# Optimization experiments

Measured on AMD Instinct MI355X. Metric: run time of the kernel, lower is better.

## Reference

```python
import math
import jax, jax.numpy as jnp
import numpy as np

N, T, D, H = 256, 128, 1024, 1024


def setup_inputs() -> dict:
    key = jax.random.key(0)
    k1, k2, k3, k4, k5 = jax.random.split(key, 5)
    x = jax.random.normal(k1, (N, T, D), dtype=jnp.float32)
    A = jax.random.normal(k2, (N, H, 4, 4), dtype=jnp.float32)
    Wx = jax.random.normal(k3, (D, 4 * H), dtype=jnp.float32) / math.sqrt(D)
    Wh = jax.random.normal(k4, (H, 4 * H), dtype=jnp.float32) / math.sqrt(H)
    Wattn = jax.random.normal(k5, (H, 4 * H), dtype=jnp.float32) / math.sqrt(H)
    b = jnp.zeros((4 * H,), dtype=jnp.float32)
    return {"x": x, "A": A, "Wx": Wx, "Wh": Wh, "Wattn": Wattn, "b": b}


def reference(x, A, Wx, Wh, Wattn, b):
    n, h = A.shape[0], A.shape[1]
    Af = A.reshape(n, h, 16)           # (N, H, 16) flattened 4x4 feature map
    h0 = Af.mean(axis=2)               # mean-pooled global feature inits h0, c0
    scale = 1.0 / math.sqrt(h)

    def step(carry, x_t):
        prev_h, prev_c = carry
        # scaled dot-product attention over 16 spatial locations
        logits = jnp.einsum("nh,nhl->nl", prev_h, Af) * scale   # (N, 16)
        w = jax.nn.softmax(logits, axis=1)
        attn = jnp.einsum("nhl,nl->nh", Af, w)                  # (N, H)
        # LSTM gates
        pre = x_t @ Wx + prev_h @ Wh + attn @ Wattn + b          # (N, 4H)
        i, f, o, g = jnp.split(pre, 4, axis=1)
        next_c = jax.nn.sigmoid(f) * prev_c + jax.nn.sigmoid(i) * jnp.tanh(g)
        next_h = jax.nn.sigmoid(o) * jnp.tanh(next_c)
        return (next_h, next_c), next_h

    xs = jnp.swapaxes(x, 0, 1)         # (T, N, D)
    _, hs = jax.lax.scan(step, (h0, h0), xs)
    return jnp.swapaxes(hs, 0, 1)      # (N, T, H)
```

## Files before the change

### kernel.cpp

```cpp
#include <hip/hip_runtime.h>
#include <hip/hip_bf16.h>

#define NB 256
#define TT 128
#define DD 1024
#define HH 1024
#define FH 4096
#define KTOT 3072

typedef __attribute__((ext_vector_type(4))) float f32x4;
typedef __attribute__((ext_vector_type(8))) short short8;

__device__ __forceinline__ unsigned short f2bf(float f) {
    union { float f; unsigned u; } v; v.f = f;
    unsigned u = v.u;
    u += 0x7FFFu + ((u >> 16) & 1u);
    return (unsigned short)(u >> 16);
}
__device__ __forceinline__ float bf2f(unsigned short u) {
    union { unsigned u; float f; } v; v.u = ((unsigned)u) << 16; return v.f;
}
__device__ __forceinline__ float sigm(float v) { return 1.f / (1.f + __expf(-v)); }
__device__ __forceinline__ float tanhf_(float v) { return 1.f - 2.f / (__expf(2.f * v) + 1.f); }

__device__ __forceinline__ void bmap(int bid, int& m0, int& j0) {
    int xx = bid & 7, yy = (bid >> 3) & 7, mt = bid >> 6;
    m0 = mt * 64;
    j0 = (xx * 8 + yy) * 16;
}

__device__ __forceinline__ short8 pack8(float4 v0, float4 v1) {
    short8 r;
    r[0] = (short)f2bf(v0.x); r[1] = (short)f2bf(v0.y);
    r[2] = (short)f2bf(v0.z); r[3] = (short)f2bf(v0.w);
    r[4] = (short)f2bf(v1.x); r[5] = (short)f2bf(v1.y);
    r[6] = (short)f2bf(v1.z); r[7] = (short)f2bf(v1.w);
    return r;
}

__global__ __launch_bounds__(256) void wt_prep(const float* __restrict__ Wx,
                                               const float* __restrict__ Wh,
                                               const float* __restrict__ Wattn,
                                               unsigned short* __restrict__ Wt) {
    __shared__ unsigned short tile[64][65];
    int k0 = blockIdx.x * 64;
    int c0 = blockIdx.y * 64;
    const float* src; int kl0;
    if (k0 < 1024)      { src = Wx;    kl0 = k0; }
    else if (k0 < 2048) { src = Wh;    kl0 = k0 - 1024; }
    else                { src = Wattn; kl0 = k0 - 2048; }
    int tid = threadIdx.x;
    int r = tid >> 2;
    int ch = (tid & 3) << 4;
    const float* p = src + (size_t)(kl0 + r) * FH + c0 + ch;
#pragma unroll
    for (int i = 0; i < 16; i += 4) {
        float4 v = *reinterpret_cast<const float4*>(p + i);
        tile[r][ch + i + 0] = f2bf(v.x);
        tile[r][ch + i + 1] = f2bf(v.y);
        tile[r][ch + i + 2] = f2bf(v.z);
        tile[r][ch + i + 3] = f2bf(v.w);
    }
    __syncthreads();
    alignas(16) unsigned short vals[16];
#pragma unroll
    for (int i = 0; i < 16; ++i) vals[i] = tile[ch + i][r];
    unsigned short* q = Wt + (size_t)(c0 + r) * KTOT + k0 + ch;
    *reinterpret_cast<uint4*>(q)     = *reinterpret_cast<uint4*>(&vals[0]);
    *reinterpret_cast<uint4*>(q + 8) = *reinterpret_cast<uint4*>(&vals[8]);
}

__global__ __launch_bounds__(256) void zero_buf(float* __restrict__ p, int n) {
    int i = blockIdx.x * 256 + threadIdx.x;
    if (i < n) p[i] = 0.f;
}

__global__ __launch_bounds__(256) void xconv(const float* __restrict__ x,
                                             unsigned short* __restrict__ xbf) {
    size_t i = ((size_t)blockIdx.x * 256 + threadIdx.x) * 8;
    float4 v0 = *reinterpret_cast<const float4*>(x + i);
    float4 v1 = *reinterpret_cast<const float4*>(x + i + 4);
    short8 p = pack8(v0, v1);
    *reinterpret_cast<short8*>(xbf + i) = p;
}

__global__ __launch_bounds__(256) void afT_prep(const float* __restrict__ A,
                                                unsigned short* __restrict__ AfT) {
    int n = blockIdx.x;
#pragma unroll
    for (int pass = 0; pass < 4; ++pass) {
        int hh = pass * 256 + threadIdx.x;
        const float4* p = reinterpret_cast<const float4*>(A + ((size_t)n * HH + hh) * 16);
        float4 a0 = p[0], a1 = p[1], a2 = p[2], a3 = p[3];
        float av[16] = {a0.x,a0.y,a0.z,a0.w, a1.x,a1.y,a1.z,a1.w,
                        a2.x,a2.y,a2.z,a2.w, a3.x,a3.y,a3.z,a3.w};
#pragma unroll
        for (int l = 0; l < 16; ++l)
            AfT[((size_t)n * 16 + l) * HH + hh] = f2bf(av[l]);
    }
}

__global__ __launch_bounds__(256) void g_gemm(const unsigned short* __restrict__ AfT,
                                              const unsigned short* __restrict__ Wt,
                                              unsigned short* __restrict__ G) {
    int n = blockIdx.y;
    int ct = blockIdx.x;
    int tid = threadIdx.x;
    int wv = tid >> 6, lane = tid & 63;
    int cw = lane & 15, k8 = (lane >> 4) << 3;
    const unsigned short* ap  = AfT + ((size_t)n * 16 + cw) * HH + k8;
    const unsigned short* bp0 = Wt + (size_t)(ct * 128 + wv * 32 + cw) * KTOT + 2048 + k8;
    const unsigned short* bp1 = Wt + (size_t)(ct * 128 + wv * 32 + 16 + cw) * KTOT + 2048 + k8;
    f32x4 acc0, acc1;
#pragma unroll
    for (int e = 0; e < 4; ++e) { acc0[e] = 0.f; acc1[e] = 0.f; }
#pragma unroll
    for (int ch = 0; ch < 32; ++ch) {
        short8 a  = *reinterpret_cast<const short8*>(ap  + ch * 32);
        short8 b0 = *reinterpret_cast<const short8*>(bp0 + ch * 32);
        short8 b1 = *reinterpret_cast<const short8*>(bp1 + ch * 32);
        acc0 = __builtin_amdgcn_mfma_f32_16x16x32_bf16(a, b0, acc0, 0, 0, 0);
        acc1 = __builtin_amdgcn_mfma_f32_16x16x32_bf16(a, b1, acc1, 0, 0, 0);
    }
    int r0 = (lane >> 4) << 2;
    int c0 = ct * 128 + wv * 32 + cw;
#pragma unroll
    for (int e = 0; e < 4; ++e) {
        int l = r0 + e;
        G[((size_t)n * FH + c0) * 16 + l]      = f2bf(acc0[e]);
        G[((size_t)n * FH + c0 + 16) * 16 + l] = f2bf(acc1[e]);
    }
}

__global__ __launch_bounds__(512) void init_kernel(const float* __restrict__ A,
                                                   float* __restrict__ c,
                                                   unsigned short* __restrict__ h0,
                                                   float* __restrict__ lg0) {
    int m0, j0; bmap(blockIdx.x, m0, j0);
    int tid = threadIdx.x;
    int r = tid >> 3, j2 = (tid & 7) * 2;
    int n = m0 + r;
    float lg[16];
#pragma unroll
    for (int l = 0; l < 16; ++l) lg[l] = 0.f;
#pragma unroll
    for (int e = 0; e < 2; ++e) {
        int j = j0 + j2 + e;
        const float4* p = reinterpret_cast<const float4*>(A + ((size_t)n * HH + j) * 16);
        float4 a0 = p[0], a1 = p[1], a2 = p[2], a3 = p[3];
        float av[16] = {a0.x,a0.y,a0.z,a0.w, a1.x,a1.y,a1.z,a1.w,
                        a2.x,a2.y,a2.z,a2.w, a3.x,a3.y,a3.z,a3.w};
        float s = 0.f;
#pragma unroll
        for (int l = 0; l < 16; ++l) s += av[l];
        float m = s * 0.0625f;
        c[(size_t)n * HH + j] = m;
        h0[(size_t)n * HH + j] = f2bf(m);
#pragma unroll
        for (int l = 0; l < 16; ++l) lg[l] += m * av[l];
    }
#pragma unroll
    for (int l = 0; l < 16; ++l) {
        lg[l] += __shfl_xor(lg[l], 1);
        lg[l] += __shfl_xor(lg[l], 2);
        lg[l] += __shfl_xor(lg[l], 4);
    }
    int l0 = (tid & 7) * 2;
    atomicAdd(&lg0[(size_t)n * 16 + l0],     lg[l0]);
    atomicAdd(&lg0[(size_t)n * 16 + l0 + 1], lg[l0 + 1]);
}

template<bool XBF>
__global__ __launch_bounds__(512)
void gemm_step(const float* __restrict__ x, const unsigned short* __restrict__ xbf,
               const unsigned short* __restrict__ hprev, unsigned short* __restrict__ hnext,
               const unsigned short* __restrict__ Wt, const unsigned short* __restrict__ G,
               const float* __restrict__ A, const float* __restrict__ bb,
               const float* __restrict__ lgcur, float* __restrict__ lgnext,
               float* __restrict__ lgz, float* __restrict__ c,
               float* __restrict__ out, int t) {
    __shared__ __attribute__((aligned(16))) char smem[131072];
    unsigned short* hsm = reinterpret_cast<unsigned short*>(smem);
    float* gsm = reinterpret_cast<float*>(smem);

    int m0, j0; bmap(blockIdx.x, m0, j0);
    int tid = threadIdx.x;
    int w = tid >> 6, lane = tid & 63;
    int wn = w & 1, wk = w >> 1;

    {
        int r = tid >> 3;
        const unsigned short* hp = hprev + (size_t)(m0 + r) * HH;
#pragma unroll
        for (int i = 0; i < 16; ++i) {
            int chunk = (tid & 7) + i * 8;
            int sw = chunk ^ (r & 7);
            *reinterpret_cast<uint4*>(&hsm[r * 1024 + sw * 8]) =
                *reinterpret_cast<const uint4*>(hp + chunk * 8);
        }
    }
    __syncthreads();

    int cw = lane & 15;
    int k8 = (lane >> 4) << 3;

    f32x4 acc[4][2];
#pragma unroll
    for (int mf = 0; mf < 4; ++mf)
#pragma unroll
        for (int fn = 0; fn < 2; ++fn)
#pragma unroll
            for (int e = 0; e < 4; ++e) acc[mf][fn][e] = 0.f;

    const unsigned short* bp[2];
#pragma unroll
    for (int fn = 0; fn < 2; ++fn) {
        int col = wn * 32 + fn * 16 + cw;
        int brow = (col >> 4) * 1024 + j0 + (col & 15);
        int kbase = (wk < 2) ? (wk * 512) : (1024 + (wk - 2) * 512);
        bp[fn] = Wt + (size_t)brow * KTOT + kbase + k8;
    }

    if (wk < 2) {
        if (XBF) {
            const unsigned short* ap[4];
#pragma unroll
            for (int mf = 0; mf < 4; ++mf)
                ap[mf] = xbf + ((size_t)(m0 + mf * 16 + cw) * TT + t) * DD + wk * 512 + k8;
#pragma unroll
            for (int ch = 0; ch < 16; ++ch) {
                short8 b0 = *reinterpret_cast<const short8*>(bp[0] + ch * 32);
                short8 b1 = *reinterpret_cast<const short8*>(bp[1] + ch * 32);
#pragma unroll
                for (int mf = 0; mf < 4; ++mf) {
                    short8 a = *reinterpret_cast<const short8*>(ap[mf] + ch * 32);
                    acc[mf][0] = __builtin_amdgcn_mfma_f32_16x16x32_bf16(a, b0, acc[mf][0], 0, 0, 0);
                    acc[mf][1] = __builtin_amdgcn_mfma_f32_16x16x32_bf16(a, b1, acc[mf][1], 0, 0, 0);
                }
            }
        } else {
            const float* ap[4];
#pragma unroll
            for (int mf = 0; mf < 4; ++mf)
                ap[mf] = x + ((size_t)(m0 + mf * 16 + cw) * TT + t) * DD + wk * 512 + k8;
#pragma unroll
            for (int ch = 0; ch < 16; ++ch) {
                short8 b0 = *reinterpret_cast<const short8*>(bp[0] + ch * 32);
                short8 b1 = *reinterpret_cast<const short8*>(bp[1] + ch * 32);
#pragma unroll
                for (int mf = 0; mf < 4; ++mf) {
                    float4 v0 = *reinterpret_cast<const float4*>(ap[mf] + ch * 32);
                    float4 v1 = *reinterpret_cast<const float4*>(ap[mf] + ch * 32 + 4);
                    short8 a = pack8(v0, v1);
                    acc[mf][0] = __builtin_amdgcn_mfma_f32_16x16x32_bf16(a, b0, acc[mf][0], 0, 0, 0);
                    acc[mf][1] = __builtin_amdgcn_mfma_f32_16x16x32_bf16(a, b1, acc[mf][1], 0, 0, 0);
                }
            }
        }
    } else {
        int kq = (wk - 2) * 512;
        int chunkBase = (kq + k8) >> 3;
#pragma unroll
        for (int ch = 0; ch < 16; ++ch) {
            short8 b0 = *reinterpret_cast<const short8*>(bp[0] + ch * 32);
            short8 b1 = *reinterpret_cast<const short8*>(bp[1] + ch * 32);
            int chunkI = chunkBase + ch * 4;
#pragma unroll
            for (int mf = 0; mf < 4; ++mf) {
                int row = mf * 16 + cw;
                int sw = chunkI ^ (row & 7);
                short8 a = *reinterpret_cast<const short8*>(&hsm[row * 1024 + sw * 8]);
                acc[mf][0] = __builtin_amdgcn_mfma_f32_16x16x32_bf16(a, b0, acc[mf][0], 0, 0, 0);
                acc[mf][1] = __builtin_amdgcn_mfma_f32_16x16x32_bf16(a, b1, acc[mf][1], 0, 0, 0);
            }
        }
    }

    __syncthreads();
    int r0 = (lane >> 4) << 2;
#pragma unroll
    for (int mf = 0; mf < 4; ++mf)
#pragma unroll
        for (int fn = 0; fn < 2; ++fn)
#pragma unroll
            for (int e = 0; e < 4; ++e)
                gsm[((size_t)wk * 64 + mf * 16 + r0 + e) * 68 + wn * 32 + fn * 16 + cw] =
                    acc[mf][fn][e];
    __syncthreads();

    int r = tid >> 3, j2 = (tid & 7) * 2;
    int n = m0 + r;

    float sm[16];
    {
        const float4* lp = reinterpret_cast<const float4*>(lgcur + (size_t)n * 16);
        float4 s0 = lp[0], s1 = lp[1], s2 = lp[2], s3 = lp[3];
        float s[16] = {s0.x,s0.y,s0.z,s0.w, s1.x,s1.y,s1.z,s1.w,
                       s2.x,s2.y,s2.z,s2.w, s3.x,s3.y,s3.z,s3.w};
        float mx = -1e30f;
#pragma unroll
        for (int l = 0; l < 16; ++l) { s[l] *= 0.03125f; mx = fmaxf(mx, s[l]); }
        float sum = 0.f;
#pragma unroll
        for (int l = 0; l < 16; ++l) { sm[l] = __expf(s[l] - mx); sum += sm[l]; }
        float inv = 1.f / sum;
#pragma unroll
        for (int l = 0; l < 16; ++l) sm[l] *= inv;
    }

    float pre[4][2];
#pragma unroll
    for (int g = 0; g < 4; ++g)
#pragma unroll
        for (int e = 0; e < 2; ++e) {
            int colL = g * 16 + j2 + e;
            float p = gsm[((size_t)0 * 64 + r) * 68 + colL]
                    + gsm[((size_t)1 * 64 + r) * 68 + colL]
                    + gsm[((size_t)2 * 64 + r) * 68 + colL]
                    + gsm[((size_t)3 * 64 + r) * 68 + colL];
            p += bb[g * HH + j0 + j2 + e];
            const unsigned short* gp = G + ((size_t)n * FH + g * HH + j0 + j2 + e) * 16;
            uint4 g0 = *reinterpret_cast<const uint4*>(gp);
            uint4 g1 = *reinterpret_cast<const uint4*>(gp + 8);
            const unsigned* gu = reinterpret_cast<const unsigned*>(&g0);
            float d = 0.f;
#pragma unroll
            for (int q = 0; q < 4; ++q) {
                d += sm[q * 2]     * bf2f((unsigned short)(gu[q] & 0xFFFF));
                d += sm[q * 2 + 1] * bf2f((unsigned short)(gu[q] >> 16));
            }
            const unsigned* gv = reinterpret_cast<const unsigned*>(&g1);
#pragma unroll
            for (int q = 0; q < 4; ++q) {
                d += sm[8 + q * 2]     * bf2f((unsigned short)(gv[q] & 0xFFFF));
                d += sm[8 + q * 2 + 1] * bf2f((unsigned short)(gv[q] >> 16));
            }
            pre[g][e] = p + d;
        }

    int j = j0 + j2;
    float2 cv = *reinterpret_cast<const float2*>(c + (size_t)n * HH + j);
    float hn[2], cn[2];
#pragma unroll
    for (int e = 0; e < 2; ++e) {
        float ig = sigm(pre[0][e]);
        float fg = sigm(pre[1][e]);
        float og = sigm(pre[2][e]);
        float gg = tanhf_(pre[3][e]);
        float cc = fg * (e ? cv.y : cv.x) + ig * gg;
        cn[e] = cc;
        hn[e] = og * tanhf_(cc);
    }
    *reinterpret_cast<float2*>(c + (size_t)n * HH + j) = make_float2(cn[0], cn[1]);
    unsigned hpack = (unsigned)f2bf(hn[0]) | ((unsigned)f2bf(hn[1]) << 16);
    *reinterpret_cast<unsigned*>(hnext + (size_t)n * HH + j) = hpack;
    *reinterpret_cast<float2*>(out + ((size_t)n * TT + t) * HH + j) = make_float2(hn[0], hn[1]);

    if ((blockIdx.x & 63) == 0) {
        int l0 = (tid & 7) * 2;
        lgz[(size_t)n * 16 + l0]     = 0.f;
        lgz[(size_t)n * 16 + l0 + 1] = 0.f;
    }

    float lg[16];
#pragma unroll
    for (int l = 0; l < 16; ++l) lg[l] = 0.f;
#pragma unroll
    for (int e = 0; e < 2; ++e) {
        const float4* p = reinterpret_cast<const float4*>(A + ((size_t)n * HH + j + e) * 16);
        float4 a0 = p[0], a1 = p[1], a2 = p[2], a3 = p[3];
        float av[16] = {a0.x,a0.y,a0.z,a0.w, a1.x,a1.y,a1.z,a1.w,
                        a2.x,a2.y,a2.z,a2.w, a3.x,a3.y,a3.z,a3.w};
        float hv = hn[e];
#pragma unroll
        for (int l = 0; l < 16; ++l) lg[l] += hv * av[l];
    }
#pragma unroll
    for (int l = 0; l < 16; ++l) {
        lg[l] += __shfl_xor(lg[l], 1);
        lg[l] += __shfl_xor(lg[l], 2);
        lg[l] += __shfl_xor(lg[l], 4);
    }
    int l0 = (tid & 7) * 2;
    atomicAdd(&lgnext[(size_t)n * 16 + l0],     lg[l0]);
    atomicAdd(&lgnext[(size_t)n * 16 + l0 + 1], lg[l0 + 1]);
}

extern "C" void kernel_launch(void* const* d_in, const int* in_sizes, int n_in,
                              void* d_out, int out_size, void* d_ws, size_t ws_size,
                              hipStream_t stream) {
    const float* x     = (const float*)d_in[0];
    const float* A     = (const float*)d_in[1];
    const float* Wx    = (const float*)d_in[2];
    const float* Wh    = (const float*)d_in[3];
    const float* Wattn = (const float*)d_in[4];
    const float* b     = (const float*)d_in[5];
    float* out = (float*)d_out;

    char* ws = (char*)d_ws;
    unsigned short* Wt   = (unsigned short*)(ws);
    unsigned short* G    = (unsigned short*)(ws + 25165824);
    unsigned short* AfT  = (unsigned short*)(ws + 58720256);
    unsigned short* hbuf = (unsigned short*)(ws + 67108864);
    float* c             = (float*)(ws + 68157440);
    float* lg            = (float*)(ws + 69206016);
    unsigned short* xbf  = (unsigned short*)(ws + 69255168);
    bool use_xbf = ws_size >= (size_t)69255168 + 67108864;

    wt_prep<<<dim3(48, 64), 256, 0, stream>>>(Wx, Wh, Wattn, Wt);
    zero_buf<<<48, 256, 0, stream>>>(lg, 3 * NB * 16);
    afT_prep<<<NB, 256, 0, stream>>>(A, AfT);
    g_gemm<<<dim3(32, NB), 256, 0, stream>>>(AfT, Wt, G);
    init_kernel<<<256, 512, 0, stream>>>(A, c, hbuf, lg);
    if (use_xbf) xconv<<<16384, 256, 0, stream>>>(x, xbf);

    for (int t = 0; t < TT; ++t) {
        const unsigned short* hp = hbuf + (size_t)(t & 1) * NB * HH;
        unsigned short* hx       = hbuf + (size_t)((t & 1) ^ 1) * NB * HH;
        float* lgc = lg + (size_t)(t % 3) * NB * 16;
        float* lgn = lg + (size_t)((t + 1) % 3) * NB * 16;
        float* lgzz = lg + (size_t)((t + 2) % 3) * NB * 16;
        if (use_xbf)
            gemm_step<true><<<256, 512, 0, stream>>>(x, xbf, hp, hx, Wt, G, A, b,
                                                     lgc, lgn, lgzz, c, out, t);
        else
            gemm_step<false><<<256, 512, 0, stream>>>(x, xbf, hp, hx, Wt, G, A, b,
                                                      lgc, lgn, lgzz, c, out, t);
    }
}
```

Before: 4.220 ms.

## Retile precompute GEMM and double per-step block threads with split-K LDS reduction

The attention-projection GEMM (g_gemm) is retiled to 128x128 output tiles per block with a 4x4 MFMA fragment grid per wave, instead of one batch row per block, so more operand data is reused per load and fewer blocks are launched. The per-timestep kernel moves from 512 to 1024 threads, each wave now covering a 32-row slice. The h operand is read directly from global memory instead of being staged in LDS, and the split-K partials are combined through a smaller LDS reduction buffer. The gate epilogue handles one column per thread. The aim is more latency hiding and shorter per-thread work on the sequential critical path, at the cost of more register pressure per block and uncached global reads of h.

```diff
diff --git a/kernel.cpp b/kernel.cpp
--- a/kernel.cpp
+++ b/kernel.cpp
@@ -103,32 +103,59 @@
 __global__ __launch_bounds__(256) void g_gemm(const unsigned short* __restrict__ AfT,
                                               const unsigned short* __restrict__ Wt,
                                               unsigned short* __restrict__ G) {
-    int n = blockIdx.y;
+    int mt = blockIdx.y;
     int ct = blockIdx.x;
     int tid = threadIdx.x;
-    int wv = tid >> 6, lane = tid & 63;
+    int w = tid >> 6, lane = tid & 63;
+    int wm = w >> 1, wn = w & 1;
     int cw = lane & 15, k8 = (lane >> 4) << 3;
-    const unsigned short* ap  = AfT + ((size_t)n * 16 + cw) * HH + k8;
-    const unsigned short* bp0 = Wt + (size_t)(ct * 128 + wv * 32 + cw) * KTOT + 2048 + k8;
-    const unsigned short* bp1 = Wt + (size_t)(ct * 128 + wv * 32 + 16 + cw) * KTOT + 2048 + k8;
-    f32x4 acc0, acc1;
-#pragma unroll
-    for (int e = 0; e < 4; ++e) { acc0[e] = 0.f; acc1[e] = 0.f; }
-#pragma unroll
+
+    const unsigned short* ap[4];
+    const unsigned short* bp[4];
+#pragma unroll
+    for (int mf = 0; mf < 4; ++mf)
+        ap[mf] = AfT + (size_t)(mt * 128 + wm * 64 + mf * 16 + cw) * HH + k8;
+#pragma unroll
+    for (int fn = 0; fn < 4; ++fn)
+        bp[fn] = Wt + (size_t)(ct * 128 + wn * 64 + fn * 16 + cw) * KTOT + 2048 + k8;
+
+    f32x4 acc[4][4];
+#pragma unroll
+    for (int mf = 0; mf < 4; ++mf)
+#pragma unroll
+        for (int fn = 0; fn < 4; ++fn)
+#pragma unroll
+            for (int e = 0; e < 4; ++e) acc[mf][fn][e] = 0.f;
+
+#pragma unroll 4
     for (int ch = 0; ch < 32; ++ch) {
-        short8 a  = *reinterpret_cast<const short8*>(ap  + ch * 32);
-        short8 b0 = *reinterpret_cast<const short8*>(bp0 + ch * 32);
-        short8 b1 = *reinterpret_cast<const short8*>(bp1 + ch * 32);
-        acc0 = __builtin_amdgcn_mfma_f32_16x16x32_bf16(a, b0, acc0, 0, 0, 0);
-        acc1 = __builtin_amdgcn_mfma_f32_16x16x32_bf16(a, b1, acc1, 0, 0, 0);
-    }
-    int r0 = (lane >> 4) << 2;
-    int c0 = ct * 128 + wv * 32 + cw;
-#pragma unroll
-    for (int e = 0; e < 4; ++e) {
-        int l = r0 + e;
-        G[((size_t)n * FH + c0) * 16 + l]      = f2bf(acc0[e]);
-        G[((size_t)n * FH + c0 + 16) * 16 + l] = f2bf(acc1[e]);
+        short8 a[4], b[4];
+#pragma unroll
+        for (int i = 0; i < 4; ++i)
+            a[i] = *reinterpret_cast<const short8*>(ap[i] + ch * 32);
+#pragma unroll
+        for (int i = 0; i < 4; ++i)
+            b[i] = *reinterpret_cast<const short8*>(bp[i] + ch * 32);
+#pragma unroll
+        for (int mf = 0; mf < 4; ++mf)
+#pragma unroll
+            for (int fn = 0; fn < 4; ++fn)
+                acc[mf][fn] = __builtin_amdgcn_mfma_f32_16x16x32_bf16(
+                    a[mf], b[fn], acc[mf][fn], 0, 0, 0);
+    }
+
+    int l0 = (lane >> 4) << 2;
+#pragma unroll
+    for (int mf = 0; mf < 4; ++mf) {
+        int n = mt * 8 + wm * 4 + mf;
+#pragma unroll
+        for (int fn = 0; fn < 4; ++fn) {
+            int cc = ct * 128 + wn * 64 + fn * 16 + cw;
+            unsigned lo = (unsigned)f2bf(acc[mf][fn][0]) | ((unsigned)f2bf(acc[mf][fn][1]) << 16);
+            unsigned hi = (unsigned)f2bf(acc[mf][fn][2]) | ((unsigned)f2bf(acc[mf][fn][3]) << 16);
+            uint2 val; val.x = lo; val.y = hi;
+            *reinterpret_cast<uint2*>(G + ((size_t)n * FH + cc) * 16 + l0) = val;
+        }
     }
 }
 
@@ -171,7 +198,7 @@
 }
 
 template<bool XBF>
-__global__ __launch_bounds__(512)
+__global__ __launch_bounds__(1024)
 void gemm_step(const float* __restrict__ x, const unsigned short* __restrict__ xbf,
                const unsigned short* __restrict__ hprev, unsigned short* __restrict__ hnext,
                const unsigned short* __restrict__ Wt, const unsigned short* __restrict__ G,
@@ -179,117 +206,115 @@
                const float* __restrict__ lgcur, float* __restrict__ lgnext,
                float* __restrict__ lgz, float* __restrict__ c,
                float* __restrict__ out, int t) {
-    __shared__ __attribute__((aligned(16))) char smem[131072];
-    unsigned short* hsm = reinterpret_cast<unsigned short*>(smem);
-    float* gsm = reinterpret_cast<float*>(smem);
-
+    __shared__ float red[2][64][68];
     int m0, j0; bmap(blockIdx.x, m0, j0);
     int tid = threadIdx.x;
     int w = tid >> 6, lane = tid & 63;
-    int wn = w & 1, wk = w >> 1;
-
-    {
-        int r = tid >> 3;
-        const unsigned short* hp = hprev + (size_t)(m0 + r) * HH;
-#pragma unroll
-        for (int i = 0; i < 16; ++i) {
-            int chunk = (tid & 7) + i * 8;
-            int sw = chunk ^ (r & 7);
-            *reinterpret_cast<uint4*>(&hsm[r * 1024 + sw * 8]) =
-                *reinterpret_cast<const uint4*>(hp + chunk * 8);
-        }
-    }
-    __syncthreads();
-
-    int cw = lane & 15;
-    int k8 = (lane >> 4) << 3;
-
-    f32x4 acc[4][2];
-#pragma unroll
-    for (int mf = 0; mf < 4; ++mf)
+    int wk = w & 3, wn = (w >> 2) & 1, wm = w >> 3;
+    int cw = lane & 15, k8 = (lane >> 4) << 3;
+
+    f32x4 acc[2][2];
+#pragma unroll
+    for (int mf = 0; mf < 2; ++mf)
 #pragma unroll
         for (int fn = 0; fn < 2; ++fn)
 #pragma unroll
             for (int e = 0; e < 4; ++e) acc[mf][fn][e] = 0.f;
 
     const unsigned short* bp[2];
+    int kbase = (wk < 2) ? wk * 512 : 1024 + (wk - 2) * 512;
 #pragma unroll
     for (int fn = 0; fn < 2; ++fn) {
         int col = wn * 32 + fn * 16 + cw;
         int brow = (col >> 4) * 1024 + j0 + (col & 15);
-        int kbase = (wk < 2) ? (wk * 512) : (1024 + (wk - 2) * 512);
         bp[fn] = Wt + (size_t)brow * KTOT + kbase + k8;
     }
 
     if (wk < 2) {
         if (XBF) {
-            const unsigned short* ap[4];
-#pragma unroll
-            for (int mf = 0; mf < 4; ++mf)
-                ap[mf] = xbf + ((size_t)(m0 + mf * 16 + cw) * TT + t) * DD + wk * 512 + k8;
-#pragma unroll
+            const unsigned short* ap[2];
+#pragma unroll
+            for (int mf = 0; mf < 2; ++mf)
+                ap[mf] = xbf + ((size_t)(m0 + wm * 32 + mf * 16 + cw) * TT + t) * DD
+                             + wk * 512 + k8;
+#pragma unroll 4
             for (int ch = 0; ch < 16; ++ch) {
+                short8 a0 = *reinterpret_cast<const short8*>(ap[0] + ch * 32);
+                short8 a1 = *reinterpret_cast<const short8*>(ap[1] + ch * 32);
                 short8 b0 = *reinterpret_cast<const short8*>(bp[0] + ch * 32);
                 short8 b1 = *reinterpret_cast<const short8*>(bp[1] + ch * 32);
-#pragma unroll
-                for (int mf = 0; mf < 4; ++mf) {
-                    short8 a = *reinterpret_cast<const short8*>(ap[mf] + ch * 32);
-                    acc[mf][0] = __builtin_amdgcn_mfma_f32_16x16x32_bf16(a, b0, acc[mf][0], 0, 0, 0);
-                    acc[mf][1] = __builtin_amdgcn_mfma_f32_16x16x32_bf16(a, b1, acc[mf][1], 0, 0, 0);
-                }
+                acc[0][0] = __builtin_amdgcn_mfma_f32_16x16x32_bf16(a0, b0, acc[0][0], 0, 0, 0);
+                acc[0][1] = __builtin_amdgcn_mfma_f32_16x16x32_bf16(a0, b1, acc[0][1], 0, 0, 0);
+                acc[1][0] = __builtin_amdgcn_mfma_f32_16x16x32_bf16(a1, b0, acc[1][0], 0, 0, 0);
+                acc[1][1] = __builtin_amdgcn_mfma_f32_16x16x32_bf16(a1, b1, acc[1][1], 0, 0, 0);
             }
         } else {
-            const float* ap[4];
-#pragma unroll
-            for (int mf = 0; mf < 4; ++mf)
-                ap[mf] = x + ((size_t)(m0 + mf * 16 + cw) * TT + t) * DD + wk * 512 + k8;
-#pragma unroll
+            const float* ap[2];
+#pragma unroll
+            for (int mf = 0; mf < 2; ++mf)
+                ap[mf] = x + ((size_t)(m0 + wm * 32 + mf * 16 + cw) * TT + t) * DD
+                           + wk * 512 + k8;
+#pragma unroll 2
             for (int ch = 0; ch < 16; ++ch) {
+                float4 u0 = *reinterpret_cast<const float4*>(ap[0] + ch * 32);
+                float4 u1 = *reinterpret_cast<const float4*>(ap[0] + ch * 32 + 4);
+                float4 v0 = *reinterpret_cast<const float4*>(ap[1] + ch * 32);
+                float4 v1 = *reinterpret_cast<const float4*>(ap[1] + ch * 32 + 4);
+                short8 a0 = pack8(u0, u1);
+                short8 a1 = pack8(v0, v1);
                 short8 b0 = *reinterpret_cast<const short8*>(bp[0] + ch * 32);
                 short8 b1 = *reinterpret_cast<const short8*>(bp[1] + ch * 32);
-#pragma unroll
-                for (int mf = 0; mf < 4; ++mf) {
-                    float4 v0 = *reinterpret_cast<const float4*>(ap[mf] + ch * 32);
-                    float4 v1 = *reinterpret_cast<const float4*>(ap[mf] + ch * 32 + 4);
-                    short8 a = pack8(v0, v1);
-                    acc[mf][0] = __builtin_amdgcn_mfma_f32_16x16x32_bf16(a, b0, acc[mf][0], 0, 0, 0);
-                    acc[mf][1] = __builtin_amdgcn_mfma_f32_16x16x32_bf16(a, b1, acc[mf][1], 0, 0, 0);
-                }
+                acc[0][0] = __builtin_amdgcn_mfma_f32_16x16x32_bf16(a0, b0, acc[0][0], 0, 0, 0);
+                acc[0][1] = __builtin_amdgcn_mfma_f32_16x16x32_bf16(a0, b1, acc[0][1], 0, 0, 0);
+                acc[1][0] = __builtin_amdgcn_mfma_f32_16x16x32_bf16(a1, b0, acc[1][0], 0, 0, 0);
+                acc[1][1] = __builtin_amdgcn_mfma_f32_16x16x32_bf16(a1, b1, acc[1][1], 0, 0, 0);
             }
         }
     } else {
-        int kq = (wk - 2) * 512;
-        int chunkBase = (kq + k8) >> 3;
-#pragma unroll
+        const unsigned short* ap[2];
+#pragma unroll
+        for (int mf = 0; mf < 2; ++mf)
+            ap[mf] = hprev + (size_t)(m0 + wm * 32 + mf * 16 + cw) * HH
+                          + (wk - 2) * 512 + k8;
+#pragma unroll 4
         for (int ch = 0; ch < 16; ++ch) {
+            short8 a0 = *reinterpret_cast<const short8*>(ap[0] + ch * 32);
+            short8 a1 = *reinterpret_cast<const short8*>(ap[1] + ch * 32);
             short8 b0 = *reinterpret_cast<const short8*>(bp[0] + ch * 32);
             short8 b1 = *reinterpret_cast<const short8*>(bp[1] + ch * 32);
-            int chunkI = chunkBase + ch * 4;
-#pragma unroll
-            for (int mf = 0; mf < 4; ++mf) {
-                int row = mf * 16 + cw;
-                int sw = chunkI ^ (row & 7);
-                short8 a = *reinterpret_cast<const short8*>(&hsm[row * 1024 + sw * 8]);
-                acc[mf][0] = __builtin_amdgcn_mfma_f32_16x16x32_bf16(a, b0, acc[mf][0], 0, 0, 0);
-                acc[mf][1] = __builtin_amdgcn_mfma_f32_16x16x32_bf16(a, b1, acc[mf][1], 0, 0, 0);
+            acc[0][0] = __builtin_amdgcn_mfma_f32_16x16x32_bf16(a0, b0, acc[0][0], 0, 0, 0);
+            acc[0][1] = __builtin_amdgcn_mfma_f32_16x16x32_bf16(a0, b1, acc[0][1], 0, 0, 0);
+            acc[1][0] = __builtin_amdgcn_mfma_f32_16x16x32_bf16(a1, b0, acc[1][0], 0, 0, 0);
+            acc[1][1] = __builtin_amdgcn_mfma_f32_16x16x32_bf16(a1, b1, acc[1][1], 0, 0, 0);
+        }
+    }
+
+    int r0 = (lane >> 4) << 2;
+    if (wk < 2) {
+#pragma unroll
+        for (int mf = 0; mf < 2; ++mf)
+#pragma unroll
+            for (int fn = 0; fn < 2; ++fn)
+                *reinterpret_cast<f32x4*>(
+                    &red[wk][wn * 32 + fn * 16 + cw][wm * 32 + mf * 16 + r0]) = acc[mf][fn];
+    }
+    __syncthreads();
+    if (wk >= 2) {
+#pragma unroll
+        for (int mf = 0; mf < 2; ++mf)
+#pragma unroll
+            for (int fn = 0; fn < 2; ++fn) {
+                float* p = &red[wk - 2][wn * 32 + fn * 16 + cw][wm * 32 + mf * 16 + r0];
+                f32x4 v = *reinterpret_cast<const f32x4*>(p);
+                v += acc[mf][fn];
+                *reinterpret_cast<f32x4*>(p) = v;
             }
-        }
-    }
-
+    }
     __syncthreads();
-    int r0 = (lane >> 4) << 2;
-#pragma unroll
-    for (int mf = 0; mf < 4; ++mf)
-#pragma unroll
-        for (int fn = 0; fn < 2; ++fn)
-#pragma unroll
-            for (int e = 0; e < 4; ++e)
-                gsm[((size_t)wk * 64 + mf * 16 + r0 + e) * 68 + wn * 32 + fn * 16 + cw] =
-                    acc[mf][fn][e];
-    __syncthreads();
-
-    int r = tid >> 3, j2 = (tid & 7) * 2;
+
+    int r = tid >> 4, j1 = tid & 15;
     int n = m0 + r;
+    int j = j0 + j1;
 
     float sm[16];
     {
@@ -308,82 +333,61 @@
         for (int l = 0; l < 16; ++l) sm[l] *= inv;
     }
 
-    float pre[4][2];
-#pragma unroll
-    for (int g = 0; g < 4; ++g)
-#pragma unroll
-        for (int e = 0; e < 2; ++e) {
-            int colL = g * 16 + j2 + e;
-            float p = gsm[((size_t)0 * 64 + r) * 68 + colL]
-                    + gsm[((size_t)1 * 64 + r) * 68 + colL]
-                    + gsm[((size_t)2 * 64 + r) * 68 + colL]
-                    + gsm[((size_t)3 * 64 + r) * 68 + colL];
-            p += bb[g * HH + j0 + j2 + e];
-            const unsigned short* gp = G + ((size_t)n * FH + g * HH + j0 + j2 + e) * 16;
-            uint4 g0 = *reinterpret_cast<const uint4*>(gp);
-            uint4 g1 = *reinterpret_cast<const uint4*>(gp + 8);
-            const unsigned* gu = reinterpret_cast<const unsigned*>(&g0);
-            float d = 0.f;
-#pragma unroll
-            for (int q = 0; q < 4; ++q) {
-                d += sm[q * 2]     * bf2f((unsigned short)(gu[q] & 0xFFFF));
-                d += sm[q * 2 + 1] * bf2f((unsigned short)(gu[q] >> 16));
-            }
-            const unsigned* gv = reinterpret_cast<const unsigned*>(&g1);
-#pragma unroll
-            for (int q = 0; q < 4; ++q) {
-                d += sm[8 + q * 2]     * bf2f((unsigned short)(gv[q] & 0xFFFF));
-                d += sm[8 + q * 2 + 1] * bf2f((unsigned short)(gv[q] >> 16));
-            }
-            pre[g][e] = p + d;
+    float pre[4];
+#pragma unroll
+    for (int g = 0; g < 4; ++g) {
+        int colL = g * 16 + j1;
+        float p = red[0][colL][r] + red[1][colL][r] + bb[g * HH + j];
+        const unsigned short* gp = G + ((size_t)n * FH + g * HH + j) * 16;
+        uint4 g0 = *reinterpret_cast<const uint4*>(gp);
+        uint4 g1 = *reinterpret_cast<const uint4*>(gp + 8);
+        const unsigned* gu = reinterpret_cast<const unsigned*>(&g0);
+        const unsigned* gv = reinterpret_cast<const unsigned*>(&g1);
+        float d = 0.f;
+#pragma unroll
+        for (int q = 0; q < 4; ++q) {
+            d += sm[q * 2]     * bf2f((unsigned short)(gu[q] & 0xFFFF));
+            d += sm[q * 2 + 1] * bf2f((unsigned short)(gu[q] >> 16));
         }
-
-    int j = j0 + j2;
-    float2 cv = *reinterpret_cast<const float2*>(c + (size_t)n * HH + j);
-    float hn[2], cn[2];
-#pragma unroll
-    for (int e = 0; e < 2; ++e) {
-        float ig = sigm(pre[0][e]);
-        float fg = sigm(pre[1][e]);
-        float og = sigm(pre[2][e]);
-        float gg = tanhf_(pre[3][e]);
-        float cc = fg * (e ? cv.y : cv.x) + ig * gg;
-        cn[e] = cc;
-        hn[e] = og * tanhf_(cc);
-    }
-    *reinterpret_cast<float2*>(c + (size_t)n * HH + j) = make_float2(cn[0], cn[1]);
-    unsigned hpack = (unsigned)f2bf(hn[0]) | ((unsigned)f2bf(hn[1]) << 16);
-    *reinterpret_cast<unsigned*>(hnext + (size_t)n * HH + j) = hpack;
-    *reinterpret_cast<float2*>(out + ((size_t)n * TT + t) * HH + j) = make_float2(hn[0], hn[1]);
-
-    if ((blockIdx.x & 63) == 0) {
-        int l0 = (tid & 7) * 2;
-        lgz[(size_t)n * 16 + l0]     = 0.f;
-        lgz[(size_t)n * 16 + l0 + 1] = 0.f;
-    }
+#pragma unroll
+        for (int q = 0; q < 4; ++q) {
+            d += sm[8 + q * 2]     * bf2f((unsigned short)(gv[q] & 0xFFFF));
+            d += sm[8 + q * 2 + 1] * bf2f((unsigned short)(gv[q] >> 16));
+        }
+        pre[g] = p + d;
+    }
+
+    float cv = c[(size_t)n * HH + j];
+    float ig = sigm(pre[0]);
+    float fg = sigm(pre[1]);
+    float og = sigm(pre[2]);
+    float gg = tanhf_(pre[3]);
+    float cn = fg * cv + ig * gg;
+    float hn = og * tanhf_(cn);
+    c[(size_t)n * HH + j] = cn;
+    hnext[(size_t)n * HH + j] = f2bf(hn);
+    out[((size_t)n * TT + t) * HH + j] = hn;
+
+    if ((blockIdx.x & 63) == 0)
+        lgz[(size_t)n * 16 + j1] = 0.f;
 
     float lg[16];
-#pragma unroll
-    for (int l = 0; l < 16; ++l) lg[l] = 0.f;
-#pragma unroll
-    for (int e = 0; e < 2; ++e) {
-        const float4* p = reinterpret_cast<const float4*>(A + ((size_t)n * HH + j + e) * 16);
+    {
+        const float4* p = reinterpret_cast<const float4*>(A + ((size_t)n * HH + j) * 16);
         float4 a0 = p[0], a1 = p[1], a2 = p[2], a3 = p[3];
-        float av[16] = {a0.x,a0.y,a0.z,a0.w, a1.x,a1.y,a1.z,a1.w,
-                        a2.x,a2.y,a2.z,a2.w, a3.x,a3.y,a3.z,a3.w};
-        float hv = hn[e];
-#pragma unroll
-        for (int l = 0; l < 16; ++l) lg[l] += hv * av[l];
+        lg[0]=hn*a0.x;  lg[1]=hn*a0.y;  lg[2]=hn*a0.z;  lg[3]=hn*a0.w;
+        lg[4]=hn*a1.x;  lg[5]=hn*a1.y;  lg[6]=hn*a1.z;  lg[7]=hn*a1.w;
+        lg[8]=hn*a2.x;  lg[9]=hn*a2.y;  lg[10]=hn*a2.z; lg[11]=hn*a2.w;
+        lg[12]=hn*a3.x; lg[13]=hn*a3.y; lg[14]=hn*a3.z; lg[15]=hn*a3.w;
     }
 #pragma unroll
     for (int l = 0; l < 16; ++l) {
         lg[l] += __shfl_xor(lg[l], 1);
         lg[l] += __shfl_xor(lg[l], 2);
         lg[l] += __shfl_xor(lg[l], 4);
-    }
-    int l0 = (tid & 7) * 2;
-    atomicAdd(&lgnext[(size_t)n * 16 + l0],     lg[l0]);
-    atomicAdd(&lgnext[(size_t)n * 16 + l0 + 1], lg[l0 + 1]);
+        lg[l] += __shfl_xor(lg[l], 8);
+    }
+    atomicAdd(&lgnext[(size_t)n * 16 + j1], lg[j1]);
 }
 
 extern "C" void kernel_launch(void* const* d_in, const int* in_sizes, int n_in,
@@ -410,21 +414,21 @@
     wt_prep<<<dim3(48, 64), 256, 0, stream>>>(Wx, Wh, Wattn, Wt);
     zero_buf<<<48, 256, 0, stream>>>(lg, 3 * NB * 16);
     afT_prep<<<NB, 256, 0, stream>>>(A, AfT);
-    g_gemm<<<dim3(32, NB), 256, 0, stream>>>(AfT, Wt, G);
+    g_gemm<<<dim3(32, 32), 256, 0, stream>>>(AfT, Wt, G);
     init_kernel<<<256, 512, 0, stream>>>(A, c, hbuf, lg);
     if (use_xbf) xconv<<<16384, 256, 0, stream>>>(x, xbf);
 
     for (int t = 0; t < TT; ++t) {
         const unsigned short* hp = hbuf + (size_t)(t & 1) * NB * HH;
         unsigned short* hx       = hbuf + (size_t)((t & 1) ^ 1) * NB * HH;
-        float* lgc = lg + (size_t)(t % 3) * NB * 16;
-        float* lgn = lg + (size_t)((t + 1) % 3) * NB * 16;
+        float* lgc  = lg + (size_t)(t % 3) * NB * 16;
+        float* lgn  = lg + (size_t)((t + 1) % 3) * NB * 16;
         float* lgzz = lg + (size_t)((t + 2) % 3) * NB * 16;
         if (use_xbf)
-            gemm_step<true><<<256, 512, 0, stream>>>(x, xbf, hp, hx, Wt, G, A, b,
-                                                     lgc, lgn, lgzz, c, out, t);
+            gemm_step<true><<<256, 1024, 0, stream>>>(x, xbf, hp, hx, Wt, G, A, b,
+                                                      lgc, lgn, lgzz, c, out, t);
         else
-            gemm_step<false><<<256, 512, 0, stream>>>(x, xbf, hp, hx, Wt, G, A, b,
-                                                      lgc, lgn, lgzz, c, out, t);
-    }
-}
+            gemm_step<false><<<256, 1024, 0, stream>>>(x, xbf, hp, hx, Wt, G, A, b,
+                                                       lgc, lgn, lgzz, c, out, t);
+    }
+}
```

Result: slower. 5.164 ms (+22.4%).
